# Performance work log

Hardware: AMD Instinct MI355X
Metric: run time of the kernel (lower is better)

Reference implementation:

```python
import jax, jax.numpy as jnp
from jax import lax
import numpy as np

S = 4          # tile_length
T = 16         # tile_size = S**2
K = 7          # length_inter_tile
NI = 49        # num_inter = K**2
CH_DE = 7      # design channels
EPS = 0.01
NEG = 0.01     # LeakyReLU default slope


def _conv(x, w, b, stride, pad):
    y = lax.conv_general_dilated(x, w, (stride, stride), [(pad, pad), (pad, pad)],
                                 dimension_numbers=('NCHW', 'OIHW', 'NCHW'))
    return y + b[None, :, None, None]


def _lrelu(x):
    return jax.nn.leaky_relu(x, NEG)


def _unfold(x, k=K):
    # torch F.unfold(x, k, padding=k//2): (B,C,H,W) -> (B, C*k*k, H*W), (c,i,j) ordering
    pad = k // 2
    B, C, H, W = x.shape
    xp = jnp.pad(x, ((0, 0), (0, 0), (pad, pad), (pad, pad)))
    cols = jnp.stack([xp[:, :, i:i + H, j:j + W] for i in range(k) for j in range(k)], axis=2)
    return cols.reshape(B, C * k * k, H * W)


def setup_inputs():
    key = jax.random.key(0)
    ks = jax.random.split(key, 16)
    B, H, W = 1, 48, 48
    CIN = 10; CF = 100; CW = 1024
    FINAL = T * T * NI  # 12544
    HALF = FINAL // 2   # 6272
    def w_init(k, shape, fan_in):
        return jax.random.normal(k, shape, jnp.float32) * np.float32(np.sqrt(2.0 / fan_in))
    return {
        'input': jax.random.normal(ks[0], (B, T, CIN, H, W), jnp.float32),
        'design': jax.random.normal(ks[1], (B, T, CH_DE, H, W), jnp.float32),
        'fw0': w_init(ks[2], (CF, CIN, 3, 3), CIN * 9),
        'fb0': jnp.zeros((CF,), jnp.float32),
        'fw_rest': w_init(ks[3], (13, CF, CF, 3, 3), CF * 9),
        'fb_rest': jnp.zeros((13, CF), jnp.float32),
        'ww0': w_init(ks[4], (CW, CF, S, S), CF * S * S),
        'wb0': jnp.zeros((CW,), jnp.float32),
        'ww_mid': w_init(ks[5], (3, CW, CW, 3, 3), CW * 9),
        'wb_mid': jnp.zeros((3, CW), jnp.float32),
        'ww1': w_init(ks[6], (HALF, CW, 1, 1), CW),
        'wb1': jnp.zeros((HALF,), jnp.float32),
        'ww2': w_init(ks[7], (FINAL, HALF, 1, 1), HALF),
        'wb2': jnp.zeros((FINAL,), jnp.float32),
    }


def reference(input, design, fw0, fb0, fw_rest, fb_rest, ww0, wb0, ww_mid, wb_mid, ww1, wb1, ww2, wb2):
    B, _, CIN, H, W = input.shape
    hw = H * W
    # domain: (B*hw, T, CH_DE)
    domain = design.transpose(0, 3, 4, 1, 2).reshape(B * hw, T, CH_DE)
    # X from unfolded design: (B*hw*NI, T, CH_DE)
    u = _unfold(design.reshape(B, T * CH_DE, H, W))
    X = u.reshape(B, T * CH_DE, NI, hw).transpose(0, 3, 2, 1).reshape(B * hw * NI, T, CH_DE)
    # make_full_res_img: stack tile (s*i + j) -> spatial offset (i, j)
    full = input.reshape(B, S, S, CIN, H, W).transpose(0, 3, 4, 1, 5, 2).reshape(B, CIN, H * S, W * S)
    # feature network: 14 conv3x3 + LeakyReLU at full res
    f = _lrelu(_conv(full, fw0, fb0, 1, 1))
    for i in range(fw_rest.shape[0]):
        f = _lrelu(_conv(f, fw_rest[i], fb_rest[i], 1, 1))
    g = _lrelu(_conv(f, ww0, wb0, S, 0))
    for i in range(ww_mid.shape[0]):
        g = _lrelu(_conv(g, ww_mid[i], wb_mid[i], 1, 1))
    g = _lrelu(_conv(g, ww1, wb1, 1, 0))
    Wmap = jnp.tanh(_conv(g, ww2, wb2, 1, 0))  # (B, NI*T*T, H, W)
    Wm = Wmap.reshape(B, NI, T, T, H, W).transpose(0, 4, 5, 1, 2, 3).reshape(B * hw * NI, T, T)
    Wm = Wm @ Wm.transpose(0, 2, 1) + jnp.eye(T, dtype=Wm.dtype)
    # normal equations
    XTW = X.transpose(0, 2, 1) @ Wm                                  # (N, CH_DE, T)
    A = (XTW @ X).reshape(B * hw, NI, CH_DE, CH_DE).sum(axis=1)
    A = A + EPS * jnp.eye(CH_DE, dtype=A.dtype)
    # all 3 color channels at once (same math as per-channel loop)
    Yu = _unfold(input[:, :, :3].reshape(B, T * 3, H, W))            # (B, T*3*NI, hw)
    Y = Yu.reshape(B, T, 3, NI, hw).transpose(0, 4, 3, 1, 2).reshape(B * hw * NI, T, 3)
    Bv = (XTW @ Y).reshape(B * hw, NI, CH_DE, 3).sum(axis=1)         # (B*hw, CH_DE, 3)
    para = jnp.linalg.solve(A, Bv)                                   # (B*hw, CH_DE, 3)
    out = (domain @ para).reshape(B, H, W, T, 3).transpose(0, 3, 4, 1, 2)
    return out
```

## Files before the change

### kernel.cpp

```cpp
#include <hip/hip_runtime.h>
#include <math.h>

#define LRELU(v) ((v) > 0.f ? (v) : 0.01f * (v))

typedef __attribute__((ext_vector_type(8))) short bf8v;
typedef __attribute__((ext_vector_type(4))) float f4v;

static __device__ __forceinline__ unsigned short f2b(float f) {
    unsigned int u = __float_as_uint(f);
    unsigned int r = (u + 0x7fffu + ((u >> 16) & 1u)) >> 16;
    return (unsigned short)r;
}

static __device__ __forceinline__ void gload16(const unsigned short* g, unsigned short* l) {
    __builtin_amdgcn_global_load_lds(
        (__attribute__((address_space(1))) void*)(g),
        (__attribute__((address_space(3))) void*)(l), 16, 0, 0);
}

__global__ __launch_bounds__(256) void k_build_full(const float* __restrict__ in,
                                                    unsigned short* __restrict__ full0p) {
    int idx = blockIdx.x * 256 + threadIdx.x;
    if (idx >= 368640) return;
    int c = idx % 10, pix = idx / 10;
    int X = pix % 192, Y = pix / 192;
    int t = (Y & 3) * 4 + (X & 3);
    int h = Y >> 2, w = X >> 2;
    int pp = (Y + 1) * 194 + (X + 1);
    full0p[(size_t)pp * 16 + c] = f2b(in[(((t * 10 + c) * 48) + h) * 48 + w]);
}

template <int C, int CP, int Q>
__global__ __launch_bounds__(256) void k_wcvt(const float* __restrict__ src,
                                              unsigned short* __restrict__ dst,
                                              int Mv, int Kp) {
    int m = blockIdx.x;
    for (int kp = threadIdx.x; kp < Kp; kp += 256) {
        int qq = kp / CP, c = kp - qq * CP;
        float v = 0.f;
        if (m < Mv && c < C && qq < Q)
            v = src[((size_t)m * C + c) * Q + qq];
        dst[(size_t)m * Kp + kp] = f2b(v);
    }
}

__global__ __launch_bounds__(256) void k_cvt_flat(const float* __restrict__ src,
                                                  unsigned short* __restrict__ dst,
                                                  size_t n) {
    size_t i = ((size_t)blockIdx.x * 256 + threadIdx.x) * 4;
    if (i >= n) return;
    float4 v = *(const float4*)(src + i);
    ushort4 o;
    o.x = f2b(v.x); o.y = f2b(v.y); o.z = f2b(v.z); o.w = f2b(v.w);
    *(ushort4*)(dst + i) = o;
}

__global__ __launch_bounds__(256) void k_im2col4(const unsigned short* __restrict__ src,
                                                 unsigned short* __restrict__ dst) {
    int p = blockIdx.x;
    int x = p % 48, y = p / 48;
    for (int kp = threadIdx.x; kp < 1600; kp += 256) {
        int qq = kp / 100, c = kp - qq * 100;
        int yy = y * 4 + (qq >> 2), xx = x * 4 + (qq & 3);
        dst[(size_t)p * 1600 + kp] = src[(size_t)((yy + 1) * 194 + (xx + 1)) * 104 + c];
    }
}

template <int ACT, int OF32, int REMAP, int SWZ>
__global__ __launch_bounds__(256) void k_gemm(
    const unsigned short* __restrict__ A, const unsigned short* __restrict__ Bt,
    const float* __restrict__ bias, void* __restrict__ outv,
    int K, int Mv, int ldout) {
    __shared__ __align__(16) unsigned short As[128 * 32];
    __shared__ __align__(16) unsigned short Bs[128 * 32];
    const int tid = threadIdx.x;
    const int lane = tid & 63;
    const int w = tid >> 6;
    const int wm = w >> 1, wn = w & 1;
    const int q = lane >> 4, ln = lane & 15;
    int bx = blockIdx.x, by = blockIdx.y;
    if (SWZ) {
        int gx = gridDim.x;
        int nwg = gx * gridDim.y;
        int lin = by * gx + bx;
        int qq = nwg >> 3, rr = nwg & 7;
        int xcd = lin & 7, idx = lin >> 3;
        int wg = (xcd < rr ? xcd * (qq + 1) : rr * (qq + 1) + (xcd - rr) * qq) + idx;
        bx = wg % gx; by = wg / gx;
    }
    const int m0 = by * 128, n0 = bx * 128;

    f4v acc[4][4];
#pragma unroll
    for (int i = 0; i < 4; ++i)
#pragma unroll
        for (int j = 0; j < 4; ++j) acc[i][j] = (f4v){0.f, 0.f, 0.f, 0.f};

    const int br0 = tid >> 2, bk0 = (tid & 3) << 3;
    const unsigned short* pA0 = A + (size_t)(m0 + br0) * K + bk0;
    const unsigned short* pA1 = pA0 + (size_t)64 * K;
    const unsigned short* pB0 = Bt + (size_t)(n0 + br0) * K + bk0;
    const unsigned short* pB1 = pB0 + (size_t)64 * K;
    unsigned short* lA0 = As + tid * 8;
    unsigned short* lA1 = As + 2048 + tid * 8;
    unsigned short* lB0 = Bs + tid * 8;
    unsigned short* lB1 = Bs + 2048 + tid * 8;
    const unsigned short* Ap2 = &As[(wm * 64 + ln) * 32 + q * 8];
    const unsigned short* Bp2 = &Bs[(wn * 64 + ln) * 32 + q * 8];

    for (int k0 = 0; k0 < K; k0 += 32) {
        gload16(pA0 + k0, lA0);
        gload16(pA1 + k0, lA1);
        gload16(pB0 + k0, lB0);
        gload16(pB1 + k0, lB1);
        __syncthreads();
        bf8v af[4], bfv[4];
#pragma unroll
        for (int i = 0; i < 4; ++i) af[i] = *(const bf8v*)(Ap2 + i * 512);
#pragma unroll
        for (int j = 0; j < 4; ++j) bfv[j] = *(const bf8v*)(Bp2 + j * 512);
#pragma unroll
        for (int i = 0; i < 4; ++i)
#pragma unroll
            for (int j = 0; j < 4; ++j)
                acc[i][j] = __builtin_amdgcn_mfma_f32_16x16x32_bf16(af[i], bfv[j], acc[i][j], 0, 0, 0);
        __syncthreads();
    }

    float* tb = ((float*)As) + w * 288;
#pragma unroll
    for (int i = 0; i < 4; ++i) {
        const int mbase = m0 + wm * 64 + i * 16;
        float bi[4];
#pragma unroll
        for (int r = 0; r < 4; ++r) {
            int mm = mbase + q * 4 + r;
            bi[r] = (mm < Mv) ? bias[mm] : 0.f;
        }
#pragma unroll
        for (int j = 0; j < 4; ++j) {
            const int nbase = n0 + wn * 64 + j * 16;
#pragma unroll
            for (int r = 0; r < 4; ++r) {
                float v = acc[i][j][r] + bi[r];
                v = ACT ? tanhf(v) : LRELU(v);
                tb[ln * 17 + q * 4 + r] = v;
            }
#pragma unroll
            for (int r = 0; r < 4; ++r) {
                float v = tb[(q * 4 + r) * 17 + ln];
                int n = nbase + q * 4 + r;
                int m = mbase + ln;
                if (m < Mv) {
                    if (REMAP == 3) {
                        int y = n / 48, x = n - y * 48;
                        size_t np = (size_t)((y + 1) * 50 + x + 1);
                        ((unsigned short*)outv)[np * (size_t)ldout + m] = f2b(v);
                    } else {
                        if (OF32) ((float*)outv)[(size_t)n * ldout + m] = v;
                        else ((unsigned short*)outv)[(size_t)n * ldout + m] = f2b(v);
                    }
                }
            }
        }
    }
}

template <int ACT, int OF32, int SWZ>
__global__ __launch_bounds__(512, 1) void k_gemm256(
    const unsigned short* __restrict__ A, const unsigned short* __restrict__ Bt,
    const float* __restrict__ bias, void* __restrict__ outv,
    int K, int Mv, int ldout) {
    __shared__ __align__(16) unsigned short As[2][16384];
    __shared__ __align__(16) unsigned short Bs[2][16384];
    const int tid = threadIdx.x;
    const int lane = tid & 63;
    const int w = tid >> 6;
    const int wm = w >> 2;
    const int wn = w & 3;
    const int q = lane >> 4, ln = lane & 15;

    int bx = blockIdx.x, by = blockIdx.y;
    if (SWZ) {
        int gx = gridDim.x;
        int nwg = gx * gridDim.y;
        int lin = by * gx + bx;
        int qq = nwg >> 3, rr = nwg & 7;
        int xcd = lin & 7, idx = lin >> 3;
        int wg = (xcd < rr ? xcd * (qq + 1) : rr * (qq + 1) + (xcd - rr) * qq) + idx;
        bx = wg % gx; by = wg / gx;
    }
    const int m0 = by * 256, n0 = bx * 256;

    f4v acc[8][4];
#pragma unroll
    for (int i = 0; i < 8; ++i)
#pragma unroll
        for (int j = 0; j < 4; ++j) acc[i][j] = (f4v){0.f, 0.f, 0.f, 0.f};

    const int srow = tid >> 3;
    const int sj = tid & 7;
    const int sjx = sj ^ (srow & 7);
    const unsigned short* gA = A + (size_t)(m0 + srow) * K + sjx * 8;
    const unsigned short* gB = Bt + (size_t)(n0 + srow) * K + sjx * 8;
    const size_t rstride = (size_t)64 * K;
    unsigned short* lA = &As[0][0] + tid * 8;
    unsigned short* lB = &Bs[0][0] + tid * 8;

#define STAGE256(buf, t)                                               \
    {                                                                  \
        const unsigned short* ga_ = gA + (size_t)(t) * 64;             \
        const unsigned short* gb_ = gB + (size_t)(t) * 64;             \
        unsigned short* la_ = lA + (buf) * 16384;                      \
        unsigned short* lb_ = lB + (buf) * 16384;                      \
        _Pragma("unroll")                                              \
        for (int r_ = 0; r_ < 4; ++r_) {                               \
            gload16(ga_ + r_ * rstride, la_ + r_ * 4096);              \
            gload16(gb_ + r_ * rstride, lb_ + r_ * 4096);              \
        }                                                              \
    }

    int aoff[8], boff[4];
#pragma unroll
    for (int mf = 0; mf < 8; ++mf) aoff[mf] = (wm * 128 + mf * 16 + ln) * 64;
#pragma unroll
    for (int nf = 0; nf < 4; ++nf) boff[nf] = (wn * 64 + nf * 16 + ln) * 64;
    const int l7 = ln & 7;
    const int koff0 = ((0 * 4 + q) ^ l7) * 8;
    const int koff1 = ((1 * 4 + q) ^ l7) * 8;

    const int NT = K >> 6;
    STAGE256(0, 0);
    STAGE256(1, 1);
    asm volatile("s_waitcnt vmcnt(8)" ::: "memory");
    __builtin_amdgcn_sched_barrier(0);
    __builtin_amdgcn_s_barrier();

    for (int t = 0; t < NT; ++t) {
        const int cur = t & 1;
        const unsigned short* as = &As[cur][0];
        const unsigned short* bs = &Bs[cur][0];
        bf8v a0[8], b0[4], a1[8], b1[4];
#pragma unroll
        for (int mf = 0; mf < 8; ++mf) a0[mf] = *(const bf8v*)&as[aoff[mf] + koff0];
#pragma unroll
        for (int nf = 0; nf < 4; ++nf) b0[nf] = *(const bf8v*)&bs[boff[nf] + koff0];
#pragma unroll
        for (int mf = 0; mf < 8; ++mf) a1[mf] = *(const bf8v*)&as[aoff[mf] + koff1];
#pragma unroll
        for (int nf = 0; nf < 4; ++nf) b1[nf] = *(const bf8v*)&bs[boff[nf] + koff1];
        __builtin_amdgcn_s_setprio(1);
#pragma unroll
        for (int mf = 0; mf < 8; ++mf)
#pragma unroll
            for (int nf = 0; nf < 4; ++nf)
                acc[mf][nf] = __builtin_amdgcn_mfma_f32_16x16x32_bf16(a0[mf], b0[nf], acc[mf][nf], 0, 0, 0);
        __builtin_amdgcn_s_setprio(0);
        asm volatile("s_waitcnt lgkmcnt(0)" ::: "memory");
        __builtin_amdgcn_sched_barrier(0);
        __builtin_amdgcn_s_barrier();
        if (t + 2 < NT) {
            STAGE256(cur, t + 2);
            asm volatile("s_waitcnt vmcnt(8)" ::: "memory");
        } else {
            asm volatile("s_waitcnt vmcnt(0)" ::: "memory");
        }
        __builtin_amdgcn_sched_barrier(0);
        __builtin_amdgcn_s_barrier();
        __builtin_amdgcn_s_setprio(1);
#pragma unroll
        for (int mf = 0; mf < 8; ++mf)
#pragma unroll
            for (int nf = 0; nf < 4; ++nf)
                acc[mf][nf] = __builtin_amdgcn_mfma_f32_16x16x32_bf16(a1[mf], b1[nf], acc[mf][nf], 0, 0, 0);
        __builtin_amdgcn_s_setprio(0);
    }
    __builtin_amdgcn_s_barrier();
#undef STAGE256

    float* tb = ((float*)&As[0][0]) + w * 288;
#pragma unroll
    for (int mf = 0; mf < 8; ++mf) {
        const int mbase = m0 + wm * 128 + mf * 16;
        float bi[4];
#pragma unroll
        for (int r = 0; r < 4; ++r) {
            int mm = mbase + q * 4 + r;
            bi[r] = (mm < Mv) ? bias[mm] : 0.f;
        }
#pragma unroll
        for (int nf = 0; nf < 4; ++nf) {
            const int nbase = n0 + wn * 64 + nf * 16;
#pragma unroll
            for (int r = 0; r < 4; ++r) {
                float v = acc[mf][nf][r] + bi[r];
                v = ACT ? tanhf(v) : LRELU(v);
                tb[ln * 17 + q * 4 + r] = v;
            }
#pragma unroll
            for (int r = 0; r < 4; ++r) {
                float v = tb[(q * 4 + r) * 17 + ln];
                int n = nbase + q * 4 + r;
                int m = mbase + ln;
                if (m < Mv) {
                    if (OF32) ((float*)outv)[(size_t)n * ldout + m] = v;
                    else ((unsigned short*)outv)[(size_t)n * ldout + m] = f2b(v);
                }
            }
        }
    }
}

template <int TAPK, int CST, int SH, int REMAP>
__global__ __launch_bounds__(256) void k_cgemm(
    const unsigned short* __restrict__ A, const unsigned short* __restrict__ Bt,
    const float* __restrict__ bias, unsigned short* __restrict__ outp,
    int Mv, int ldout) {
    __shared__ __align__(16) unsigned short As[128 * 32];
    __shared__ __align__(16) unsigned short Bs[128 * 32];
    const int tid = threadIdx.x;
    const int lane = tid & 63;
    const int w = tid >> 6;
    const int wm = w >> 1, wn = w & 1;
    const int q = lane >> 4, ln = lane & 15;
    const int m0 = blockIdx.y * 128, n0 = blockIdx.x * 128;
    const int KA = 9 * TAPK;

    f4v acc[4][4];
#pragma unroll
    for (int i = 0; i < 4; ++i)
#pragma unroll
        for (int j = 0; j < 4; ++j) acc[i][j] = (f4v){0.f, 0.f, 0.f, 0.f};

    const int br0 = tid >> 2, bk0 = (tid & 3) << 3;
    const unsigned short* pA0 = A + (size_t)(m0 + br0) * KA + bk0;
    const unsigned short* pA1 = pA0 + (size_t)64 * KA;
    unsigned short* lA0 = As + tid * 8;
    unsigned short* lA1 = As + 2048 + tid * 8;
    unsigned short* lB0 = Bs + tid * 8;
    unsigned short* lB1 = Bs + 2048 + tid * 8;
    const unsigned short* Ap2 = &As[(wm * 64 + ln) * 32 + q * 8];
    const unsigned short* Bp2 = &Bs[(wn * 64 + ln) * 32 + q * 8];

#pragma unroll
    for (int tap = 0; tap < 9; ++tap) {
        const int sh = (tap / 3 - 1) * SH + (tap % 3 - 1);
        const unsigned short* pB0 = Bt + (long)(n0 + br0 + sh) * CST + bk0;
        const unsigned short* pB1 = pB0 + (long)64 * CST;
        const int kab = tap * TAPK;
        for (int kk = 0; kk < TAPK; kk += 32) {
            gload16(pA0 + kab + kk, lA0);
            gload16(pA1 + kab + kk, lA1);
            gload16(pB0 + kk, lB0);
            gload16(pB1 + kk, lB1);
            __syncthreads();
            bf8v af[4], bfv[4];
#pragma unroll
            for (int i = 0; i < 4; ++i) af[i] = *(const bf8v*)(Ap2 + i * 512);
#pragma unroll
            for (int j = 0; j < 4; ++j) bfv[j] = *(const bf8v*)(Bp2 + j * 512);
#pragma unroll
            for (int i = 0; i < 4; ++i)
#pragma unroll
                for (int j = 0; j < 4; ++j)
                    acc[i][j] = __builtin_amdgcn_mfma_f32_16x16x32_bf16(af[i], bfv[j], acc[i][j], 0, 0, 0);
            __syncthreads();
        }
    }

    float* tb = ((float*)As) + w * 288;
#pragma unroll
    for (int i = 0; i < 4; ++i) {
        const int mbase = m0 + wm * 64 + i * 16;
        float bi[4];
#pragma unroll
        for (int r = 0; r < 4; ++r) {
            int mm = mbase + q * 4 + r;
            bi[r] = (mm < Mv) ? bias[mm] : 0.f;
        }
#pragma unroll
        for (int j = 0; j < 4; ++j) {
            const int nbase = n0 + wn * 64 + j * 16;
#pragma unroll
            for (int r = 0; r < 4; ++r) {
                float v = acc[i][j][r] + bi[r];
                v = LRELU(v);
                tb[ln * 17 + q * 4 + r] = v;
            }
#pragma unroll
            for (int r = 0; r < 4; ++r) {
                float v = tb[(q * 4 + r) * 17 + ln];
                int n = nbase + q * 4 + r;
                int m = mbase + ln;
                if (m < Mv) {
                    if (REMAP == 1) {
                        int y = n / 194, x = n - y * 194;
                        bool z = (n >= 37636) || y == 0 || y >= 193 || x == 0 || x >= 193;
                        outp[(size_t)n * ldout + m] = f2b(z ? 0.f : v);
                    } else if (REMAP == 2) {
                        int y = n / 50, x = n - y * 50;
                        bool z = (n >= 2500) || y == 0 || y >= 49 || x == 0 || x >= 49;
                        outp[(size_t)n * ldout + m] = f2b(z ? 0.f : v);
                    } else if (REMAP == 4) {
                        int y = n / 50, x = n - y * 50;
                        if (n < 2500 && y >= 1 && y <= 48 && x >= 1 && x <= 48)
                            outp[(size_t)((y - 1) * 48 + (x - 1)) * ldout + m] = f2b(v);
                    }
                }
            }
        }
    }
}

template <int ACT, int OF32, int AF32>
__global__ __launch_bounds__(256) void k_gemm_f32a(
    const void* __restrict__ Ain, const unsigned short* __restrict__ Bt,
    const float* __restrict__ bias, void* __restrict__ outv,
    int K, int Mv, int ldout) {
    __shared__ __align__(16) unsigned short As[128 * 40];
    __shared__ __align__(16) unsigned short Bs[128 * 40];
    const int tid = threadIdx.x;
    const int lane = tid & 63;
    const int w = tid >> 6;
    const int wm = w >> 1, wn = w & 1;
    const int q = lane >> 4, ln = lane & 15;
    const int m0 = blockIdx.y * 128, n0 = blockIdx.x * 128;

    f4v acc[4][4];
#pragma unroll
    for (int i = 0; i < 4; ++i)
#pragma unroll
        for (int j = 0; j < 4; ++j) acc[i][j] = (f4v){0.f, 0.f, 0.f, 0.f};

    const int br0 = tid >> 2, bk0 = (tid & 3) << 3;
    const int br1 = br0 + 64;
    const int bl0 = br0 * 40 + bk0, bl1 = br1 * 40 + bk0;
    const unsigned short* pB0 = Bt + (size_t)(n0 + br0) * K + bk0;
    const unsigned short* pB1 = Bt + (size_t)(n0 + br1) * K + bk0;

    const unsigned short* Ab = (const unsigned short*)Ain;
    const float* Af = (const float*)Ain;
    const unsigned short* pA0 = Ab + (size_t)(m0 + br0) * K + bk0;
    const unsigned short* pA1 = Ab + (size_t)(m0 + br1) * K + bk0;
    const int fr = tid >> 3, fk = (tid & 7) << 2;
    const float* pF = Af + (size_t)(m0 + fr) * K + fk;

    for (int k0 = 0; k0 < K; k0 += 32) {
        if (AF32) {
#pragma unroll
            for (int jj = 0; jj < 4; ++jj) {
                float4 v = *(const float4*)(pF + (size_t)jj * 32 * K + k0);
                unsigned int lo = ((unsigned)f2b(v.y) << 16) | f2b(v.x);
                unsigned int hi = ((unsigned)f2b(v.w) << 16) | f2b(v.z);
                *(uint2*)&As[(fr + jj * 32) * 40 + fk] = make_uint2(lo, hi);
            }
        } else {
            uint4 a0 = *(const uint4*)(pA0 + k0);
            uint4 a1 = *(const uint4*)(pA1 + k0);
            *(uint4*)&As[bl0] = a0;
            *(uint4*)&As[bl1] = a1;
        }
        uint4 b0 = *(const uint4*)(pB0 + k0);
        uint4 b1 = *(const uint4*)(pB1 + k0);
        *(uint4*)&Bs[bl0] = b0;
        *(uint4*)&Bs[bl1] = b1;
        __syncthreads();
        const unsigned short* Ap2 = &As[(wm * 64 + ln) * 40 + q * 8];
        const unsigned short* Bp2 = &Bs[(wn * 64 + ln) * 40 + q * 8];
        bf8v af[4], bfv[4];
#pragma unroll
        for (int i = 0; i < 4; ++i) af[i] = *(const bf8v*)(Ap2 + i * 640);
#pragma unroll
        for (int j = 0; j < 4; ++j) bfv[j] = *(const bf8v*)(Bp2 + j * 640);
#pragma unroll
        for (int i = 0; i < 4; ++i)
#pragma unroll
            for (int j = 0; j < 4; ++j)
                acc[i][j] = __builtin_amdgcn_mfma_f32_16x16x32_bf16(af[i], bfv[j], acc[i][j], 0, 0, 0);
        __syncthreads();
    }

    float* tb = ((float*)As) + w * 288;
#pragma unroll
    for (int i = 0; i < 4; ++i) {
        const int mbase = m0 + wm * 64 + i * 16;
        float bi[4];
#pragma unroll
        for (int r = 0; r < 4; ++r) {
            int mm = mbase + q * 4 + r;
            bi[r] = (mm < Mv) ? bias[mm] : 0.f;
        }
#pragma unroll
        for (int j = 0; j < 4; ++j) {
            const int nbase = n0 + wn * 64 + j * 16;
#pragma unroll
            for (int r = 0; r < 4; ++r) {
                float v = acc[i][j][r] + bi[r];
                v = ACT ? tanhf(v) : LRELU(v);
                tb[ln * 17 + q * 4 + r] = v;
            }
#pragma unroll
            for (int r = 0; r < 4; ++r) {
                float v = tb[(q * 4 + r) * 17 + ln];
                size_t n = nbase + q * 4 + r;
                int m = mbase + ln;
                if (m < Mv) {
                    if (OF32) ((float*)outv)[n * (size_t)ldout + m] = v;
                    else ((unsigned short*)outv)[n * (size_t)ldout + m] = f2b(v);
                }
            }
        }
    }
}

__global__ __launch_bounds__(256) void k_solve(const float* __restrict__ WmT,
                                               const float* __restrict__ design,
                                               const float* __restrict__ input,
                                               float* __restrict__ out) {
    const int p = blockIdx.x;
    const int h = p / 48, wpx = p % 48;
    const int tid = threadIdx.x;
    __shared__ float Msh[16 * 17];
    __shared__ float Gsh[16 * 17];
    __shared__ float Xsh[16 * 8];
    __shared__ float Ysh[16 * 4];
    __shared__ float XTWsh[7 * 17];
    __shared__ float Aacc[49];
    __shared__ float Bacc[21];
    __shared__ float parash[21];

    if (tid < 49) Aacc[tid] = 0.f;
    if (tid >= 64 && tid < 85) Bacc[tid - 64] = 0.f;
    __syncthreads();

    const float* wrow = WmT + (size_t)p * 12544;
    for (int ni = 0; ni < 49; ++ni) {
        {
            int t1 = tid >> 4, t2 = tid & 15;
            Msh[t1 * 17 + t2] = wrow[ni * 256 + tid];
        }
        int sy = h + ni / 7 - 3, sx = wpx + ni % 7 - 3;
        bool inb = (sy >= 0 && sy < 48 && sx >= 0 && sx < 48);
        if (tid < 112) {
            int t = tid / 7, c = tid - t * 7;
            Xsh[t * 8 + c] = inb ? design[(size_t)(t * 7 + c) * 2304 + sy * 48 + sx] : 0.f;
        } else if (tid >= 128 && tid < 176) {
            int l = tid - 128;
            int t = l / 3, r = l - t * 3;
            Ysh[t * 4 + r] = inb ? input[(size_t)(t * 10 + r) * 2304 + sy * 48 + sx] : 0.f;
        }
        __syncthreads();
        {
            int t1 = tid >> 4, t2 = tid & 15;
            float s = (t1 == t2) ? 1.f : 0.f;
#pragma unroll
            for (int k = 0; k < 16; ++k) s += Msh[t1 * 17 + k] * Msh[t2 * 17 + k];
            Gsh[t1 * 17 + t2] = s;
        }
        __syncthreads();
        if (tid < 112) {
            int c = tid >> 4, t2 = tid & 15;
            float s = 0.f;
#pragma unroll
            for (int t1 = 0; t1 < 16; ++t1) s += Xsh[t1 * 8 + c] * Gsh[t1 * 17 + t2];
            XTWsh[c * 17 + t2] = s;
        }
        __syncthreads();
        if (tid < 49) {
            int c1 = tid / 7, c2 = tid - c1 * 7;
            float s = 0.f;
#pragma unroll
            for (int t = 0; t < 16; ++t) s += XTWsh[c1 * 17 + t] * Xsh[t * 8 + c2];
            Aacc[tid] += s;
        } else if (tid >= 64 && tid < 85) {
            int l = tid - 64;
            int c = l / 3, r = l - c * 3;
            float s = 0.f;
#pragma unroll
            for (int t = 0; t < 16; ++t) s += XTWsh[c * 17 + t] * Ysh[t * 4 + r];
            Bacc[l] += s;
        }
        __syncthreads();
    }

    if (tid == 0) {
        float Mg[7][10];
#pragma unroll
        for (int i = 0; i < 7; ++i) {
#pragma unroll
            for (int j = 0; j < 7; ++j) Mg[i][j] = Aacc[i * 7 + j] + ((i == j) ? 0.01f : 0.f);
#pragma unroll
            for (int r = 0; r < 3; ++r) Mg[i][7 + r] = Bacc[i * 3 + r];
        }
#pragma unroll
        for (int kk = 0; kk < 7; ++kk) {
            float inv = 1.f / Mg[kk][kk];
#pragma unroll
            for (int j = 0; j < 10; ++j) Mg[kk][j] *= inv;
#pragma unroll
            for (int i = 0; i < 7; ++i) {
                if (i == kk) continue;
                float f = Mg[i][kk];
#pragma unroll
                for (int j = 0; j < 10; ++j) Mg[i][j] -= f * Mg[kk][j];
            }
        }
#pragma unroll
        for (int c = 0; c < 7; ++c)
#pragma unroll
            for (int r = 0; r < 3; ++r) parash[c * 3 + r] = Mg[c][7 + r];
    }
    __syncthreads();

    if (tid < 48) {
        int t = tid / 3, r = tid - t * 3;
        float s = 0.f;
#pragma unroll
        for (int c = 0; c < 7; ++c)
            s += design[(size_t)(t * 7 + c) * 2304 + p] * parash[c * 3 + r];
        out[(size_t)tid * 2304 + p] = s;
    }
}

extern "C" void kernel_launch(void* const* d_in, const int* in_sizes, int n_in,
                              void* d_out, int out_size, void* d_ws, size_t ws_size,
                              hipStream_t stream) {
    const float* input   = (const float*)d_in[0];
    const float* design  = (const float*)d_in[1];
    const float* fw0     = (const float*)d_in[2];
    const float* fb0     = (const float*)d_in[3];
    const float* fw_rest = (const float*)d_in[4];
    const float* fb_rest = (const float*)d_in[5];
    const float* ww0     = (const float*)d_in[6];
    const float* wb0     = (const float*)d_in[7];
    const float* ww_mid  = (const float*)d_in[8];
    const float* wb_mid  = (const float*)d_in[9];
    const float* ww1     = (const float*)d_in[10];
    const float* wb1     = (const float*)d_in[11];
    const float* ww2     = (const float*)d_in[12];
    const float* wb2     = (const float*)d_in[13];
    float* out = (float*)d_out;
    float* ws = (float*)d_ws;

    float* WmT = ws;
    unsigned short* full0p = (unsigned short*)(ws + 40000);
    unsigned short* actPA  = (unsigned short*)(ws + 350000);
    unsigned short* actPB  = (unsigned short*)(ws + 2330000);
    unsigned short* fw0c   = (unsigned short*)(ws + 4310000);
    unsigned short* fwrb   = (unsigned short*)(ws + 4330000);
    unsigned short* ww0b   = (unsigned short*)(ws + 5290000);
    unsigned short* col4   = (unsigned short*)(ws + 6110000);
    unsigned short* gPA    = (unsigned short*)(ws + 7960000);
    unsigned short* gPB    = (unsigned short*)(ws + 9340000);
    unsigned short* wmb    = (unsigned short*)(ws + 10720000);
    unsigned short* gcmp   = (unsigned short*)(ws + 15440000);
    unsigned short* g1     = (unsigned short*)(ws + 28901376);
    unsigned short* ww1b   = (unsigned short*)(ws + 36126720);
    const size_t WS_BASE_F = 39337984ull;
    unsigned short* ww2b   = (unsigned short*)(ws + WS_BASE_F);
    unsigned short* ww1bp  = (unsigned short*)(ws + 59006976);
    const size_t NEED_BIG = 59006976ull + 3276800ull;

    hipMemsetAsync(full0p, 0, (size_t)37956 * 16 * 2, stream);
    hipMemsetAsync(actPA, 0, (size_t)37956 * 104 * 2, stream);
    hipMemsetAsync(actPB, 0, (size_t)37956 * 104 * 2, stream);
    hipMemsetAsync(gPA, 0, (size_t)2688 * 1024 * 2, stream);
    hipMemsetAsync(gPB, 0, (size_t)2688 * 1024 * 2, stream);

    const size_t haveF = ws_size / 4;
    const bool big = (haveF >= NEED_BIG) && (haveF >= WS_BASE_F + 39337984ull);

    k_wcvt<10, 32, 9><<<128, 256, 0, stream>>>(fw0, fw0c, 100, 288);
    for (int i = 0; i < 13; ++i)
        k_wcvt<100, 128, 9><<<128, 256, 0, stream>>>(fw_rest + (size_t)i * 90000,
                                                     fwrb + (size_t)i * 147456, 100, 1152);
    k_wcvt<100, 100, 16><<<1024, 256, 0, stream>>>(ww0, ww0b, 1024, 1600);
    if (big)
        k_wcvt<1024, 1024, 1><<<6400, 256, 0, stream>>>(ww1, ww1bp, 6272, 1024);
    else
        k_wcvt<1024, 1024, 1><<<6272, 256, 0, stream>>>(ww1, ww1b, 6272, 1024);

    k_build_full<<<1440, 256, 0, stream>>>(input, full0p);
    k_cgemm<32, 16, 194, 1><<<dim3(295, 1), 256, 0, stream>>>(fw0c, full0p, fb0, actPA, 100, 104);
    unsigned short* src = actPA;
    unsigned short* dst = actPB;
    for (int i = 0; i < 13; ++i) {
        k_cgemm<128, 104, 194, 1><<<dim3(295, 1), 256, 0, stream>>>(
            fwrb + (size_t)i * 147456, src, fb_rest + i * 100, dst, 100, 104);
        unsigned short* t = src; src = dst; dst = t;
    }

    k_im2col4<<<2304, 256, 0, stream>>>(src, col4);
    k_gemm<0, 0, 3, 0><<<dim3(18, 8), 256, 0, stream>>>(ww0b, col4, wb0, gPA, 1600, 1024, 1024);

    k_wcvt<1024, 1024, 9><<<1024, 256, 0, stream>>>(ww_mid, wmb, 1024, 9216);
    k_cgemm<1024, 1024, 50, 2><<<dim3(20, 8), 256, 0, stream>>>(wmb, gPA, wb_mid, gPB, 1024, 1024);
    k_wcvt<1024, 1024, 9><<<1024, 256, 0, stream>>>(ww_mid + (size_t)9437184, wmb, 1024, 9216);
    k_cgemm<1024, 1024, 50, 2><<<dim3(20, 8), 256, 0, stream>>>(wmb, gPB, wb_mid + 1024, gPA, 1024, 1024);
    k_wcvt<1024, 1024, 9><<<1024, 256, 0, stream>>>(ww_mid + (size_t)2 * 9437184, wmb, 1024, 9216);
    k_cgemm<1024, 1024, 50, 4><<<dim3(20, 8), 256, 0, stream>>>(wmb, gPA, wb_mid + 2048, gcmp, 1024, 1024);

    if (big) {
        k_gemm256<0, 0, 1><<<dim3(9, 25), 512, 0, stream>>>(ww1bp, gcmp, wb1, g1, 1024, 6272, 6272);
        k_cvt_flat<<<76832, 256, 0, stream>>>(ww2, ww2b, (size_t)12544 * 6272);
        k_gemm256<1, 1, 1><<<dim3(9, 49), 512, 0, stream>>>(ww2b, g1, wb2, WmT, 6272, 12544, 12544);
    } else {
        k_gemm<0, 0, 0, 1><<<dim3(18, 49), 256, 0, stream>>>(ww1b, gcmp, wb1, g1, 1024, 6272, 6272);
        k_gemm_f32a<1, 1, 1><<<dim3(18, 98), 256, 0, stream>>>(ww2, g1, wb2, WmT, 6272, 12544, 12544);
    }

    k_solve<<<2304, 256, 0, stream>>>(WmT, design, input, out);
}
```

Before: 2.362 ms.

## Software-pipeline LDS reads in gemm256 and use 64-row tiles for mid convs

The k_gemm256 main loop is restructured so the second half-K MFMA block of one iteration overlaps the LDS fragment loads for the next tile, with a peeled prologue and epilogue. This is meant to hide LDS read latency behind matrix-core work. Separately, a new k_cgemm64 kernel with 64x128 tiles replaces k_cgemm for the three 1024-channel 3x3 convs, doubling the grid to 320 blocks to fill more CUs. The new kernel has no double buffering and syncs twice per K step, which may limit its throughput.

```diff
diff --git a/kernel.cpp b/kernel.cpp
--- a/kernel.cpp
+++ b/kernel.cpp
@@ -236,15 +236,54 @@
     __builtin_amdgcn_sched_barrier(0);
     __builtin_amdgcn_s_barrier();
 
-    for (int t = 0; t < NT; ++t) {
+    bf8v a0[8], b0[4], a1[8], b1[4];
+
+    {
+        const unsigned short* as = &As[0][0];
+        const unsigned short* bs = &Bs[0][0];
+#pragma unroll
+        for (int mf = 0; mf < 8; ++mf) a0[mf] = *(const bf8v*)&as[aoff[mf] + koff0];
+#pragma unroll
+        for (int nf = 0; nf < 4; ++nf) b0[nf] = *(const bf8v*)&bs[boff[nf] + koff0];
+#pragma unroll
+        for (int mf = 0; mf < 8; ++mf) a1[mf] = *(const bf8v*)&as[aoff[mf] + koff1];
+#pragma unroll
+        for (int nf = 0; nf < 4; ++nf) b1[nf] = *(const bf8v*)&bs[boff[nf] + koff1];
+        __builtin_amdgcn_s_setprio(1);
+#pragma unroll
+        for (int mf = 0; mf < 8; ++mf)
+#pragma unroll
+            for (int nf = 0; nf < 4; ++nf)
+                acc[mf][nf] = __builtin_amdgcn_mfma_f32_16x16x32_bf16(a0[mf], b0[nf], acc[mf][nf], 0, 0, 0);
+        __builtin_amdgcn_s_setprio(0);
+        asm volatile("s_waitcnt lgkmcnt(0)" ::: "memory");
+        __builtin_amdgcn_sched_barrier(0);
+        __builtin_amdgcn_s_barrier();
+        if (2 < NT) {
+            STAGE256(0, 2);
+            asm volatile("s_waitcnt vmcnt(8)" ::: "memory");
+        } else {
+            asm volatile("s_waitcnt vmcnt(0)" ::: "memory");
+        }
+        __builtin_amdgcn_sched_barrier(0);
+        __builtin_amdgcn_s_barrier();
+    }
+
+    for (int t = 1; t < NT; ++t) {
         const int cur = t & 1;
         const unsigned short* as = &As[cur][0];
         const unsigned short* bs = &Bs[cur][0];
-        bf8v a0[8], b0[4], a1[8], b1[4];
 #pragma unroll
         for (int mf = 0; mf < 8; ++mf) a0[mf] = *(const bf8v*)&as[aoff[mf] + koff0];
 #pragma unroll
         for (int nf = 0; nf < 4; ++nf) b0[nf] = *(const bf8v*)&bs[boff[nf] + koff0];
+        __builtin_amdgcn_s_setprio(1);
+#pragma unroll
+        for (int mf = 0; mf < 8; ++mf)
+#pragma unroll
+            for (int nf = 0; nf < 4; ++nf)
+                acc[mf][nf] = __builtin_amdgcn_mfma_f32_16x16x32_bf16(a1[mf], b1[nf], acc[mf][nf], 0, 0, 0);
+        __builtin_amdgcn_s_setprio(0);
 #pragma unroll
         for (int mf = 0; mf < 8; ++mf) a1[mf] = *(const bf8v*)&as[aoff[mf] + koff1];
 #pragma unroll
@@ -267,14 +306,14 @@
         }
         __builtin_amdgcn_sched_barrier(0);
         __builtin_amdgcn_s_barrier();
-        __builtin_amdgcn_s_setprio(1);
-#pragma unroll
-        for (int mf = 0; mf < 8; ++mf)
-#pragma unroll
-            for (int nf = 0; nf < 4; ++nf)
-                acc[mf][nf] = __builtin_amdgcn_mfma_f32_16x16x32_bf16(a1[mf], b1[nf], acc[mf][nf], 0, 0, 0);
-        __builtin_amdgcn_s_setprio(0);
-    }
+    }
+    __builtin_amdgcn_s_setprio(1);
+#pragma unroll
+    for (int mf = 0; mf < 8; ++mf)
+#pragma unroll
+        for (int nf = 0; nf < 4; ++nf)
+            acc[mf][nf] = __builtin_amdgcn_mfma_f32_16x16x32_bf16(a1[mf], b1[nf], acc[mf][nf], 0, 0, 0);
+    __builtin_amdgcn_s_setprio(0);
     __builtin_amdgcn_s_barrier();
 #undef STAGE256
 
@@ -398,6 +437,99 @@
                         bool z = (n >= 37636) || y == 0 || y >= 193 || x == 0 || x >= 193;
                         outp[(size_t)n * ldout + m] = f2b(z ? 0.f : v);
                     } else if (REMAP == 2) {
+                        int y = n / 50, x = n - y * 50;
+                        bool z = (n >= 2500) || y == 0 || y >= 49 || x == 0 || x >= 49;
+                        outp[(size_t)n * ldout + m] = f2b(z ? 0.f : v);
+                    } else if (REMAP == 4) {
+                        int y = n / 50, x = n - y * 50;
+                        if (n < 2500 && y >= 1 && y <= 48 && x >= 1 && x <= 48)
+                            outp[(size_t)((y - 1) * 48 + (x - 1)) * ldout + m] = f2b(v);
+                    }
+                }
+            }
+        }
+    }
+}
+
+template <int TAPK, int CST, int SH, int REMAP>
+__global__ __launch_bounds__(256) void k_cgemm64(
+    const unsigned short* __restrict__ A, const unsigned short* __restrict__ Bt,
+    const float* __restrict__ bias, unsigned short* __restrict__ outp,
+    int Mv, int ldout) {
+    __shared__ __align__(16) unsigned short As[64 * 32];
+    __shared__ __align__(16) unsigned short Bs[128 * 32];
+    const int tid = threadIdx.x;
+    const int lane = tid & 63;
+    const int wn = tid >> 6;
+    const int q = lane >> 4, ln = lane & 15;
+    const int m0 = blockIdx.y * 64, n0 = blockIdx.x * 128;
+    const int KA = 9 * TAPK;
+
+    f4v acc[4][2];
+#pragma unroll
+    for (int i = 0; i < 4; ++i)
+#pragma unroll
+        for (int j = 0; j < 2; ++j) acc[i][j] = (f4v){0.f, 0.f, 0.f, 0.f};
+
+    const int br0 = tid >> 2, bk0 = (tid & 3) << 3;
+    const unsigned short* pA0 = A + (size_t)(m0 + br0) * KA + bk0;
+    unsigned short* lA0 = As + tid * 8;
+    unsigned short* lB0 = Bs + tid * 8;
+    unsigned short* lB1 = Bs + 2048 + tid * 8;
+    const unsigned short* Ap2 = &As[ln * 32 + q * 8];
+    const unsigned short* Bp2 = &Bs[(wn * 32 + ln) * 32 + q * 8];
+
+#pragma unroll
+    for (int tap = 0; tap < 9; ++tap) {
+        const int sh = (tap / 3 - 1) * SH + (tap % 3 - 1);
+        const unsigned short* pB0 = Bt + (long)(n0 + br0 + sh) * CST + bk0;
+        const unsigned short* pB1 = pB0 + (long)64 * CST;
+        const int kab = tap * TAPK;
+        for (int kk = 0; kk < TAPK; kk += 32) {
+            gload16(pA0 + kab + kk, lA0);
+            gload16(pB0 + kk, lB0);
+            gload16(pB1 + kk, lB1);
+            __syncthreads();
+            bf8v af[4], bfv[2];
+#pragma unroll
+            for (int i = 0; i < 4; ++i) af[i] = *(const bf8v*)(Ap2 + i * 512);
+#pragma unroll
+            for (int j = 0; j < 2; ++j) bfv[j] = *(const bf8v*)(Bp2 + j * 512);
+#pragma unroll
+            for (int i = 0; i < 4; ++i)
+#pragma unroll
+                for (int j = 0; j < 2; ++j)
+                    acc[i][j] = __builtin_amdgcn_mfma_f32_16x16x32_bf16(af[i], bfv[j], acc[i][j], 0, 0, 0);
+            __syncthreads();
+        }
+    }
+
+    float* tb = ((float*)Bs) + wn * 288;
+#pragma unroll
+    for (int i = 0; i < 4; ++i) {
+        const int mbase = m0 + i * 16;
+        float bi[4];
+#pragma unroll
+        for (int r = 0; r < 4; ++r) {
+            int mm = mbase + q * 4 + r;
+            bi[r] = (mm < Mv) ? bias[mm] : 0.f;
+        }
+#pragma unroll
+        for (int j = 0; j < 2; ++j) {
+            const int nbase = n0 + wn * 32 + j * 16;
+#pragma unroll
+            for (int r = 0; r < 4; ++r) {
+                float v = acc[i][j][r] + bi[r];
+                v = LRELU(v);
+                tb[ln * 17 + q * 4 + r] = v;
+            }
+#pragma unroll
+            for (int r = 0; r < 4; ++r) {
+                float v = tb[(q * 4 + r) * 17 + ln];
+                int n = nbase + q * 4 + r;
+                int m = mbase + ln;
+                if (m < Mv) {
+                    if (REMAP == 2) {
                         int y = n / 50, x = n - y * 50;
                         bool z = (n >= 2500) || y == 0 || y >= 49 || x == 0 || x >= 49;
                         outp[(size_t)n * ldout + m] = f2b(z ? 0.f : v);
@@ -694,11 +826,11 @@
     k_gemm<0, 0, 3, 0><<<dim3(18, 8), 256, 0, stream>>>(ww0b, col4, wb0, gPA, 1600, 1024, 1024);
 
     k_wcvt<1024, 1024, 9><<<1024, 256, 0, stream>>>(ww_mid, wmb, 1024, 9216);
-    k_cgemm<1024, 1024, 50, 2><<<dim3(20, 8), 256, 0, stream>>>(wmb, gPA, wb_mid, gPB, 1024, 1024);
+    k_cgemm64<1024, 1024, 50, 2><<<dim3(20, 16), 256, 0, stream>>>(wmb, gPA, wb_mid, gPB, 1024, 1024);
     k_wcvt<1024, 1024, 9><<<1024, 256, 0, stream>>>(ww_mid + (size_t)9437184, wmb, 1024, 9216);
-    k_cgemm<1024, 1024, 50, 2><<<dim3(20, 8), 256, 0, stream>>>(wmb, gPB, wb_mid + 1024, gPA, 1024, 1024);
+    k_cgemm64<1024, 1024, 50, 2><<<dim3(20, 16), 256, 0, stream>>>(wmb, gPB, wb_mid + 1024, gPA, 1024, 1024);
     k_wcvt<1024, 1024, 9><<<1024, 256, 0, stream>>>(ww_mid + (size_t)2 * 9437184, wmb, 1024, 9216);
-    k_cgemm<1024, 1024, 50, 4><<<dim3(20, 8), 256, 0, stream>>>(wmb, gPA, wb_mid + 2048, gcmp, 1024, 1024);
+    k_cgemm64<1024, 1024, 50, 4><<<dim3(20, 16), 256, 0, stream>>>(wmb, gPA, wb_mid + 2048, gcmp, 1024, 1024);
 
     if (big) {
         k_gemm256<0, 0, 1><<<dim3(9, 25), 512, 0, stream>>>(ww1bp, gcmp, wb1, g1, 1024, 6272, 6272);
```

New measurement: 2.325 ms. Within noise of the previous version (-1.6%).
